# Optimization experiments

Measured on AMD Instinct MI355X. Metric: run time of the kernel, lower is better.

Reference implementation:

```python
import jax, jax.numpy as jnp
import numpy as np

EPS_NORM = 1e-7   # Normalize module eps (added to norm)
EPS_COS = 1e-8    # torch F.cosine_similarity default eps (clamped denom)


def _normalize(x):
    # Normalize(power=2): x / (||x||_2 + 1e-7), norm over dim 1
    n = jnp.sqrt(jnp.sum(x * x, axis=1, keepdims=True))
    return x / (n + EPS_NORM)


def _cos_sim_matrix(f):
    # pairwise cosine similarity, matching torch cosine_similarity semantics:
    # (f_i . f_j) / max(||f_i|| * ||f_j||, eps)
    n = jnp.linalg.norm(f, axis=1)            # [N]
    denom = jnp.maximum(n[:, None] * n[None, :], EPS_COS)
    return (f @ f.T) / denom                   # [N, N]


def setup_inputs() -> dict:
    key = jax.random.key(0)
    kq, kk = jax.random.split(key)
    N, D = 4096, 1024
    feat_q = jax.random.normal(kq, (N, D), dtype=jnp.float32)
    feat_k = jax.random.normal(kk, (N, D), dtype=jnp.float32)
    return {"feat_q": feat_q, "feat_k": feat_k}


def reference(feat_q, feat_k):
    q = _normalize(feat_q)
    k = jax.lax.stop_gradient(_normalize(feat_k))  # feat_k.detach()
    Sq = _cos_sim_matrix(q)   # [N, N]
    Sk = _cos_sim_matrix(k)   # [N, N]
    N = feat_q.shape[0]
    off_diag = ~jnp.eye(N, dtype=bool)
    diff2 = (Sq - Sk) ** 2
    # mean over the N*(N-1) off-diagonal (i != j) pairs
    loss = jnp.sum(jnp.where(off_diag, diff2, 0.0)) / (N * (N - 1))
    return loss
```

## Files before the change

kernel.cpp:

```cpp
#include <hip/hip_runtime.h>
#include <stdint.h>

#define N_ROWS 4096
#define DIMS   1024
#define BM 128
#define BK 128
#define TG 16
#define NTRI 136
#define KSPLIT 4
#define KCHUNK 1024

typedef __attribute__((ext_vector_type(2))) long longx2;
typedef __attribute__((ext_vector_type(4))) float f32x4;

__device__ __forceinline__ unsigned short f2bf(float f) {
  union { float f; unsigned int u; } c; c.f = f;
  unsigned int u = c.u;
  return (unsigned short)((u + 0x7fffu + ((u >> 16) & 1u)) >> 16);
}
__device__ __forceinline__ float bf2f(unsigned short v) {
  union { float f; unsigned int u; } c; c.u = ((unsigned int)v) << 16;
  return c.f;
}
__device__ __forceinline__ unsigned int pk4_fp8(float a, float b, float c, float d) {
  int v = __builtin_amdgcn_cvt_pk_fp8_f32(a, b, 0, false);
  v = __builtin_amdgcn_cvt_pk_fp8_f32(c, d, v, true);
  return (unsigned int)v;
}
__device__ __forceinline__ void async_cp16(const unsigned char* g, void* lds) {
  __builtin_amdgcn_global_load_lds(
      (const __attribute__((address_space(1))) void*)g,
      (__attribute__((address_space(3))) void*)lds, 16, 0, 0);
}

__global__ __launch_bounds__(256) void rownorm_kernel(
    const float* __restrict__ fq, const float* __restrict__ fk,
    float* __restrict__ invq, float* __restrict__ invk, float* __restrict__ out) {
  if (blockIdx.x == 0 && blockIdx.y == 0 && threadIdx.x == 0) out[0] = 0.0f;
  const int w = threadIdx.x >> 6, lane = threadIdx.x & 63;
  const int row = blockIdx.x * 4 + w;
  const float* src = blockIdx.y ? fk : fq;
  float* dst = blockIdx.y ? invk : invq;
  const float4* s4 = (const float4*)(src + (size_t)row * DIMS);
  float ss = 0.0f;
  #pragma unroll
  for (int s = 0; s < 4; ++s) {
    float4 v = s4[lane + 64 * s];
    ss += v.x * v.x + v.y * v.y + v.z * v.z + v.w * v.w;
  }
  #pragma unroll
  for (int off = 32; off > 0; off >>= 1) ss += __shfl_xor(ss, off);
  if (lane == 0) dst[row] = 1.0f / sqrtf(ss);
}

__global__ __launch_bounds__(256) void transpose_scale_kernel(
    const float* __restrict__ fq, const float* __restrict__ fk,
    const float* __restrict__ invq, const float* __restrict__ invk,
    unsigned char* __restrict__ Mt) {
  __shared__ unsigned short tile[64][260];
  const int i0 = blockIdx.x * 256;
  const int a0 = blockIdx.y * 64;
  const int w = threadIdx.x >> 6, lane = threadIdx.x & 63;
  const float* src;
  const float* inv;
  int acol;
  if (a0 < DIMS) { src = fq; inv = invq; acol = a0 + lane; }
  else           { src = fk; inv = invk; acol = a0 - DIMS + lane; }

  for (int c0 = 0; c0 < 64; c0 += 4) {
    ushort4 v;
    unsigned short* vp = (unsigned short*)&v;
    #pragma unroll
    for (int c = 0; c < 4; ++c) {
      const int i = i0 + w * 64 + c0 + c;
      vp[c] = f2bf(src[(size_t)i * DIMS + acol] * inv[i]);
    }
    *(ushort4*)&tile[lane][w * 64 + c0] = v;
  }
  __syncthreads();
  const int il = (lane * 4) & 127;
  const int blk = (i0 + lane * 4) >> 7;
  const int q = (il >> 3) & 3, s0 = (il >> 5) & 1, s1 = (il >> 6) & 1;
  const int pos = q * 32 + s1 * 16 + s0 * 8 + (il & 7);
  #pragma unroll
  for (int r = 0; r < 16; ++r) {
    const int al = w * 16 + r;
    ushort4 v = *(const ushort4*)&tile[al][lane * 4];
    const unsigned int p8 = pk4_fp8(bf2f(v.x), bf2f(v.y), bf2f(v.z), bf2f(v.w));
    *(unsigned int*)(Mt + (size_t)(a0 + al) * N_ROWS + blk * 128 + pos) = p8;
  }
}

__global__ __launch_bounds__(256, 2) void gram_partial_kernel(
    const unsigned char* __restrict__ Mt, unsigned short* __restrict__ Gp) {
  __shared__ __align__(16) char smem[2 * BM * BK];

  const int t = blockIdx.x >> 2;
  const int kc = blockIdx.x & 3;
  int I = 0, rem = t;
  while (rem >= (TG - I)) { rem -= (TG - I); ++I; }
  const int J = I + rem;

  const int tid = threadIdx.x, w = tid >> 6, lane = tid & 63;

  const int isB = w >> 1;
  const int rblk = isB ? J : I;
  const int rl = lane >> 3;
  const int cl = (lane & 7) ^ rl;
  const bool skipStage = (isB && I == J);
  const unsigned char* gsrc0 =
      Mt + (size_t)(rblk * BM + (w & 1) * 64 + rl) * N_ROWS + kc * KCHUNK + cl * 16;
  char* ldsBase = smem + isB * 16384 + (w & 1) * 8192;
  const int bOff = (I == J) ? 0 : 16384;

  const int wr = w >> 1, wc = w & 1;
  const int ml = lane & 15, quad = lane >> 4;
  const int ar0 = wr * 64, bc0 = wc * 64;

  f32x4 acc[4][4] = {};

  for (int kk = 0; kk < KCHUNK; kk += BK) {
    if (!skipStage) {
      const unsigned char* g = gsrc0 + kk;
      #pragma unroll
      for (int s = 0; s < 8; ++s)
        async_cp16(g + (size_t)s * 8 * N_ROWS, ldsBase + s * 1024);
    }
    __syncthreads();
    longx2 a[4][2], b[4][2];
    #pragma unroll
    for (int i = 0; i < 4; ++i) {
      const int ra = (ar0 + i * 16 + ml) * BK;
      const int rb = (bc0 + i * 16 + ml) * BK;
      #pragma unroll
      for (int s1 = 0; s1 < 2; ++s1) {
        const int slot = ((quad * 2 + s1) ^ (ml & 7)) * 16;
        a[i][s1] = *(const longx2*)(smem + ra + slot);
        b[i][s1] = *(const longx2*)(smem + bOff + rb + slot);
      }
    }
    #pragma unroll
    for (int s1 = 0; s1 < 2; ++s1)
      #pragma unroll
      for (int h = 0; h < 2; ++h)
        #pragma unroll
        for (int i = 0; i < 4; ++i)
          #pragma unroll
          for (int j = 0; j < 4; ++j)
            acc[i][j] = __builtin_amdgcn_mfma_f32_16x16x32_fp8_fp8(
                a[i][s1][h], b[j][s1][h], acc[i][j], 0, 0, 0);
    __syncthreads();
  }

  unsigned short* slab = Gp + (size_t)blockIdx.x * (BM * BM) + w * 4096;
  #pragma unroll
  for (int i = 0; i < 4; ++i)
    #pragma unroll
    for (int j = 0; j < 4; ++j) {
      ushort4 o;
      o.x = f2bf(acc[i][j][0]); o.y = f2bf(acc[i][j][1]);
      o.z = f2bf(acc[i][j][2]); o.w = f2bf(acc[i][j][3]);
      *(ushort4*)(slab + (i * 4 + j) * 256 + lane * 4) = o;
    }
}

__global__ __launch_bounds__(256) void square_reduce_kernel(
    const unsigned short* __restrict__ Gp, float* __restrict__ out) {
  __shared__ float wsum[4];
  const int t = blockIdx.x >> 3;
  const int seg = blockIdx.x & 7;
  int I = 0, rem = t;
  while (rem >= (TG - I)) { rem -= (TG - I); ++I; }
  const int J = I + rem;

  const unsigned short* base =
      Gp + (size_t)t * (KSPLIT * BM * BM) + seg * 2048 + threadIdx.x * 8;
  float s[8] = {0, 0, 0, 0, 0, 0, 0, 0};
  #pragma unroll
  for (int kc = 0; kc < KSPLIT; ++kc) {
    const ushort4 v0 = *(const ushort4*)(base + kc * (BM * BM));
    const ushort4 v1 = *(const ushort4*)(base + kc * (BM * BM) + 4);
    s[0] += bf2f(v0.x); s[1] += bf2f(v0.y); s[2] += bf2f(v0.z); s[3] += bf2f(v0.w);
    s[4] += bf2f(v1.x); s[5] += bf2f(v1.y); s[6] += bf2f(v1.z); s[7] += bf2f(v1.w);
  }
  float local = 0.0f;
  #pragma unroll
  for (int x = 0; x < 8; ++x) local += s[x] * s[x];

  const float sgn = ((I < 8) == (J < 8)) ? 1.0f : -1.0f;
  local *= (I == J ? 1.0f : 2.0f) * sgn;

  #pragma unroll
  for (int off = 32; off > 0; off >>= 1) local += __shfl_xor(local, off);
  const int w = threadIdx.x >> 6, lane = threadIdx.x & 63;
  if (lane == 0) wsum[w] = local;
  __syncthreads();
  if (threadIdx.x == 0) {
    const float ts = wsum[0] + wsum[1] + wsum[2] + wsum[3];
    atomicAdd(out, ts * (1.0f / 16773120.0f));
  }
}

extern "C" void kernel_launch(void* const* d_in, const int* in_sizes, int n_in,
                              void* d_out, int out_size, void* d_ws, size_t ws_size,
                              hipStream_t stream) {
  const float* fq = (const float*)d_in[0];
  const float* fk = (const float*)d_in[1];
  float* invq = (float*)d_ws;
  float* invk = invq + N_ROWS;
  unsigned char* Mt = (unsigned char*)d_ws + 32768;
  unsigned short* Gp = (unsigned short*)(Mt + (size_t)2048 * N_ROWS);
  float* out = (float*)d_out;

  rownorm_kernel<<<dim3(N_ROWS / 4, 2), 256, 0, stream>>>(fq, fk, invq, invk, out);
  transpose_scale_kernel<<<dim3(16, 32), 256, 0, stream>>>(fq, fk, invq, invk, Mt);
  gram_partial_kernel<<<NTRI * KSPLIT, 256, 0, stream>>>(Mt, Gp);
  square_reduce_kernel<<<NTRI * 8, 256, 0, stream>>>(Gp, out);
}
```

Baseline: 116.5 us.

## Use 128x256 grouped Gram tiles with 8-way K split and masked diagonal reduction

```diff
diff --git a/kernel.cpp b/kernel.cpp
--- a/kernel.cpp
+++ b/kernel.cpp
@@ -3,14 +3,15 @@
 
 #define N_ROWS 4096
 #define DIMS   1024
-#define BM 128
-#define BK 128
-#define TG 16
-#define NTRI 136
-#define KSPLIT 4
-#define KCHUNK 1024
+#define TGR    16
+#define NJOBT  72
+#define KSPLIT 8
+#define KCHUNK 512
+#define BKB    128
+#define NITER  4
 
 typedef __attribute__((ext_vector_type(2))) long longx2;
+typedef __attribute__((ext_vector_type(8))) unsigned short ushort8;
 typedef __attribute__((ext_vector_type(4))) float f32x4;
 
 __device__ __forceinline__ unsigned short f2bf(float f) {
@@ -80,8 +81,8 @@
   __syncthreads();
   const int il = (lane * 4) & 127;
   const int blk = (i0 + lane * 4) >> 7;
-  const int q = (il >> 3) & 3, s0 = (il >> 5) & 1, s1 = (il >> 6) & 1;
-  const int pos = q * 32 + s1 * 16 + s0 * 8 + (il & 7);
+  const int q = (il >> 3) & 3, s0b = (il >> 5) & 1, s1b = (il >> 6) & 1;
+  const int pos = q * 32 + s1b * 16 + s0b * 8 + (il & 7);
   #pragma unroll
   for (int r = 0; r < 16; ++r) {
     const int al = w * 16 + r;
@@ -91,53 +92,60 @@
   }
 }
 
-__global__ __launch_bounds__(256, 2) void gram_partial_kernel(
+__global__ __launch_bounds__(256, 2) void gram_grouped_kernel(
     const unsigned char* __restrict__ Mt, unsigned short* __restrict__ Gp) {
-  __shared__ __align__(16) char smem[2 * BM * BK];
-
-  const int t = blockIdx.x >> 2;
-  const int kc = blockIdx.x & 3;
-  int I = 0, rem = t;
-  while (rem >= (TG - I)) { rem -= (TG - I); ++I; }
-  const int J = I + rem;
+  __shared__ __align__(16) char smem[384 * 128];
+
+  const int job = blockIdx.x;
+  const int t = job >> 3;
+  const int kc = job & 7;
+  int R = 0, rem = t;
+  while (rem >= 8 - (R >> 1)) { rem -= 8 - (R >> 1); ++R; }
+  const int C = (R >> 1) + rem;
+  const bool strad = ((R >> 1) == C);
 
   const int tid = threadIdx.x, w = tid >> 6, lane = tid & 63;
-
-  const int isB = w >> 1;
-  const int rblk = isB ? J : I;
   const int rl = lane >> 3;
   const int cl = (lane & 7) ^ rl;
-  const bool skipStage = (isB && I == J);
-  const unsigned char* gsrc0 =
-      Mt + (size_t)(rblk * BM + (w & 1) * 64 + rl) * N_ROWS + kc * KCHUNK + cl * 16;
-  char* ldsBase = smem + isB * 16384 + (w & 1) * 8192;
-  const int bOff = (I == J) ? 0 : 16384;
-
-  const int wr = w >> 1, wc = w & 1;
+
   const int ml = lane & 15, quad = lane >> 4;
-  const int ar0 = wr * 64, bc0 = wc * 64;
-
-  f32x4 acc[4][4] = {};
-
-  for (int kk = 0; kk < KCHUNK; kk += BK) {
-    if (!skipStage) {
-      const unsigned char* g = gsrc0 + kk;
-      #pragma unroll
-      for (int s = 0; s < 8; ++s)
-        async_cp16(g + (size_t)s * 8 * N_ROWS, ldsBase + s * 1024);
+  const int ar0 = (w >> 1) * 64, bc0 = (w & 1) * 128;
+  const char* aBase = strad ? (smem + 16384 + (R & 1) * 16384) : smem;
+  const char* bBase = smem + 16384;
+
+  f32x4 acc[4][8] = {};
+
+  for (int it = 0; it < NITER; ++it) {
+    const size_t kof = (size_t)kc * KCHUNK + (size_t)it * BKB + cl * 16;
+    if (!strad) {
+      #pragma unroll
+      for (int g = 0; g < 12; ++g) {
+        const int rho = w * 96 + g * 8;
+        const int grow = (rho < 128) ? (R * 128 + rho) : (C * 256 + rho - 128);
+        async_cp16(Mt + (size_t)(grow + rl) * N_ROWS + kof,
+                   smem + rho * 128 + lane * 16);
+      }
+    } else {
+      #pragma unroll
+      for (int g = 0; g < 8; ++g) {
+        const int rho = 128 + w * 64 + g * 8;
+        const int grow = C * 256 + rho - 128;
+        async_cp16(Mt + (size_t)(grow + rl) * N_ROWS + kof,
+                   smem + rho * 128 + lane * 16);
+      }
     }
     __syncthreads();
-    longx2 a[4][2], b[4][2];
-    #pragma unroll
-    for (int i = 0; i < 4; ++i) {
-      const int ra = (ar0 + i * 16 + ml) * BK;
-      const int rb = (bc0 + i * 16 + ml) * BK;
-      #pragma unroll
-      for (int s1 = 0; s1 < 2; ++s1) {
-        const int slot = ((quad * 2 + s1) ^ (ml & 7)) * 16;
-        a[i][s1] = *(const longx2*)(smem + ra + slot);
-        b[i][s1] = *(const longx2*)(smem + bOff + rb + slot);
-      }
+
+    longx2 a[4][2], b[8][2];
+    #pragma unroll
+    for (int s1 = 0; s1 < 2; ++s1) {
+      const int slot = ((quad * 2 + s1) ^ (ml & 7)) * 16;
+      #pragma unroll
+      for (int i = 0; i < 4; ++i)
+        a[i][s1] = *(const longx2*)(aBase + (ar0 + i * 16 + ml) * 128 + slot);
+      #pragma unroll
+      for (int j = 0; j < 8; ++j)
+        b[j][s1] = *(const longx2*)(bBase + (bc0 + j * 16 + ml) * 128 + slot);
     }
     #pragma unroll
     for (int s1 = 0; s1 < 2; ++s1)
@@ -146,49 +154,66 @@
         #pragma unroll
         for (int i = 0; i < 4; ++i)
           #pragma unroll
-          for (int j = 0; j < 4; ++j)
+          for (int j = 0; j < 8; ++j)
             acc[i][j] = __builtin_amdgcn_mfma_f32_16x16x32_fp8_fp8(
                 a[i][s1][h], b[j][s1][h], acc[i][j], 0, 0, 0);
     __syncthreads();
   }
 
-  unsigned short* slab = Gp + (size_t)blockIdx.x * (BM * BM) + w * 4096;
+  unsigned short* slab = Gp + (size_t)job * 32768 + w * 8192;
   #pragma unroll
   for (int i = 0; i < 4; ++i)
     #pragma unroll
-    for (int j = 0; j < 4; ++j) {
+    for (int j = 0; j < 8; ++j) {
       ushort4 o;
       o.x = f2bf(acc[i][j][0]); o.y = f2bf(acc[i][j][1]);
       o.z = f2bf(acc[i][j][2]); o.w = f2bf(acc[i][j][3]);
-      *(ushort4*)(slab + (i * 4 + j) * 256 + lane * 4) = o;
+      *(ushort4*)(slab + (i * 8 + j) * 256 + lane * 4) = o;
     }
 }
 
 __global__ __launch_bounds__(256) void square_reduce_kernel(
     const unsigned short* __restrict__ Gp, float* __restrict__ out) {
   __shared__ float wsum[4];
-  const int t = blockIdx.x >> 3;
-  const int seg = blockIdx.x & 7;
-  int I = 0, rem = t;
-  while (rem >= (TG - I)) { rem -= (TG - I); ++I; }
-  const int J = I + rem;
-
-  const unsigned short* base =
-      Gp + (size_t)t * (KSPLIT * BM * BM) + seg * 2048 + threadIdx.x * 8;
+  const int t = blockIdx.x >> 4;
+  const int seg = blockIdx.x & 15;
+  int R = 0, rem = t;
+  while (rem >= 8 - (R >> 1)) { rem -= 8 - (R >> 1); ++R; }
+  const int C = (R >> 1) + rem;
+  const bool fullAbove = (R < 2 * C);
+
+  const int off0 = seg * 2048 + threadIdx.x * 8;
+  const unsigned short* base = Gp + (size_t)t * (KSPLIT * 32768) + off0;
   float s[8] = {0, 0, 0, 0, 0, 0, 0, 0};
   #pragma unroll
   for (int kc = 0; kc < KSPLIT; ++kc) {
-    const ushort4 v0 = *(const ushort4*)(base + kc * (BM * BM));
-    const ushort4 v1 = *(const ushort4*)(base + kc * (BM * BM) + 4);
-    s[0] += bf2f(v0.x); s[1] += bf2f(v0.y); s[2] += bf2f(v0.z); s[3] += bf2f(v0.w);
-    s[4] += bf2f(v1.x); s[5] += bf2f(v1.y); s[6] += bf2f(v1.z); s[7] += bf2f(v1.w);
-  }
+    const ushort8 v = *(const ushort8*)(base + kc * 32768);
+    #pragma unroll
+    for (int x = 0; x < 8; ++x) s[x] += bf2f(v[x]);
+  }
+
   float local = 0.0f;
-  #pragma unroll
-  for (int x = 0; x < 8; ++x) local += s[x] * s[x];
-
-  const float sgn = ((I < 8) == (J < 8)) ? 1.0f : -1.0f;
-  local *= (I == J ? 1.0f : 2.0f) * sgn;
+  if (fullAbove) {
+    #pragma unroll
+    for (int x = 0; x < 8; ++x) local += 2.0f * s[x] * s[x];
+  } else {
+    #pragma unroll
+    for (int x = 0; x < 8; ++x) {
+      const int off = off0 + x;
+      const int wv = off >> 13;
+      const int rm = off & 8191;
+      const int fi = rm >> 8;
+      const int l4 = rm & 255;
+      const int ln = l4 >> 2, p = l4 & 3;
+      const int r = (wv >> 1) * 64 + (fi >> 3) * 16 + (ln >> 4) * 4 + p;
+      const int c = (wv & 1) * 128 + (fi & 7) * 16 + (ln & 15);
+      const int gr = R * 128 + r, gc = C * 256 + c;
+      const float wgt = (gr < gc) ? 2.0f : (gr == gc ? 1.0f : 0.0f);
+      local += wgt * s[x] * s[x];
+    }
+  }
+  const float sgn = ((R < 8) == (C < 4)) ? 1.0f : -1.0f;
+  local *= sgn;
 
   #pragma unroll
   for (int off = 32; off > 0; off >>= 1) local += __shfl_xor(local, off);
@@ -214,6 +239,6 @@
 
   rownorm_kernel<<<dim3(N_ROWS / 4, 2), 256, 0, stream>>>(fq, fk, invq, invk, out);
   transpose_scale_kernel<<<dim3(16, 32), 256, 0, stream>>>(fq, fk, invq, invk, Mt);
-  gram_partial_kernel<<<NTRI * KSPLIT, 256, 0, stream>>>(Mt, Gp);
-  square_reduce_kernel<<<NTRI * 8, 256, 0, stream>>>(Gp, out);
-}
+  gram_grouped_kernel<<<NJOBT * KSPLIT, 256, 0, stream>>>(Mt, Gp);
+  square_reduce_kernel<<<NJOBT * 16, 256, 0, stream>>>(Gp, out);
+}
```

Result: slower. 134.0 us (+15.0%).
